# Kernel tuning notes

Measured on AMD Instinct MI355X. Metric: run time of the kernel, lower is better.

Reference implementation:

```python
import jax, jax.numpy as jnp
import numpy as np

N, H, CIN, C, G = 50000, 16, 256, 256, 8
CPG = C // G          # 32 channels per group
CR = C // 4           # delta MLP hidden (delta_reduction=4)

def _lrelu(x):
    return jax.nn.leaky_relu(x, 0.1)

def setup_inputs() -> dict:
    key = jax.random.key(0)
    ks = jax.random.split(key, 16)
    def lin(k, fin, fout):
        return jax.random.normal(k, (fin, fout), jnp.float32) / np.sqrt(fin)
    return {
        'q_pts': jax.random.normal(ks[0], (N, 3), jnp.float32),
        's_pts': jax.random.normal(ks[1], (N, 3), jnp.float32),
        's_feats': jax.random.normal(ks[2], (N, CIN), jnp.float32),
        'neighb_inds': jax.random.randint(ks[3], (N, H), 0, N, jnp.int64),
        'Wq': lin(ks[4], CIN, C), 'bq': jnp.zeros((C,), jnp.float32),
        'Wk': lin(ks[5], CIN, C), 'bk': jnp.zeros((C,), jnp.float32),
        'Wv': lin(ks[6], CIN, C), 'bv': jnp.zeros((C,), jnp.float32),
        'Wd1': lin(ks[7], 3, CR), 'bd1': jnp.zeros((CR,), jnp.float32),
        'Wd2': lin(ks[8], CR, C), 'bd2': jnp.zeros((C,), jnp.float32),
        'Wa1': lin(ks[9], C, CPG), 'ba1': jnp.zeros((CPG,), jnp.float32),
        'Wa2': lin(ks[10], CPG, CPG), 'ba2': jnp.zeros((CPG,), jnp.float32),
    }

def reference(q_pts, s_pts, s_feats, neighb_inds,
              Wq, bq, Wk, bk, Wv, bv,
              Wd1, bd1, Wd2, bd2, Wa1, ba1, Wa2, ba2):
    # q/k/v projections  (N, C)
    v = s_feats @ Wv + bv
    k = s_feats @ Wk + bk
    q = s_feats @ Wq + bq
    # gather neighbor features (all indices < N, shadow mask is a no-op)
    nv = v[neighb_inds]                 # (N, H, C)
    nk = k[neighb_inds]                 # (N, H, C)
    # relative positions (torch.no_grad in source)
    rel = s_pts[neighb_inds] - q_pts[:, None, :]   # (N, H, 3)
    # delta MLP: 3 -> C/4 -> C (UnaryBlock + Linear, norm='none')
    geom = _lrelu(rel @ Wd1 + bd1) @ Wd2 + bd2     # (N, H, C)
    # geom_mode='sub': v-branch and qk-branch both subtract geom encodings
    nv = nv - geom
    # source always enters strided branch (s_pts padded before the check);
    # stride_mode='nearest' -> q feature of the first neighbor
    qf = q[neighb_inds[:, 0]]                      # (N, C)
    qk = qf[:, None, :] - nk - geom                # (N, H, C)
    # alpha MLP: NormBlock(id) + act, Linear C->CpG + act, Linear CpG->CpG
    a = _lrelu(qk)
    a = _lrelu(a @ Wa1 + ba1)
    a = a @ Wa2 + ba2                              # (N, H, CpG)
    attn = jax.nn.softmax(a, axis=1)               # softmax over neighbors
    # grouped weighted aggregation: C split as (CpG, G), attn broadcast over G
    out = (nv.reshape(N, H, CPG, G) * attn[..., None]).sum(axis=1)
    return out.reshape(N, C)
```

## Files before the change

### kernel.cpp

```cpp
#include <hip/hip_runtime.h>
#include <cstdint>
#include <cstddef>

#define N_PTS 50000
#define H 16
#define CIN 256
#define C 256
#define CPG 32
#define CR 64

typedef short bf16x8 __attribute__((ext_vector_type(8)));
typedef float f32x4 __attribute__((ext_vector_type(4)));

__device__ __forceinline__ unsigned short f2bf(float f) {
    unsigned int u = __float_as_uint(f);
    u += 0x7fff + ((u >> 16) & 1);
    return (unsigned short)(u >> 16);
}
__device__ __forceinline__ float bf2f(unsigned short s) {
    return __uint_as_float(((unsigned int)s) << 16);
}

__global__ __launch_bounds__(256) void prep_all(
    const float* __restrict__ feats,
    const float* __restrict__ Wq, const float* __restrict__ Wk,
    const float* __restrict__ Wv,
    const float* __restrict__ Wd2, const float* __restrict__ Wa1,
    const float* __restrict__ Wa2,
    unsigned short* __restrict__ A_bf16,
    unsigned short* __restrict__ gemmFrags,
    unsigned short* __restrict__ attnFrags)
{
    int bid = blockIdx.x;
    if (bid < 6250) {
        size_t i = ((size_t)bid * 256 + threadIdx.x) * 8;
        float4 f0 = *(const float4*)&feats[i];
        float4 f1 = *(const float4*)&feats[i + 4];
        unsigned short t[8] = {f2bf(f0.x), f2bf(f0.y), f2bf(f0.z), f2bf(f0.w),
                               f2bf(f1.x), f2bf(f1.y), f2bf(f1.z), f2bf(f1.w)};
        *(bf16x8*)&A_bf16[i] = *(bf16x8*)t;
    } else if (bid < 6346) {
        int t = (bid - 6250) * 256 + threadIdx.x;
        int lane = t & 63;
        int f = t >> 6;
        int ntg = f % 48;
        const float* W = ntg < 16 ? Wq : (ntg < 32 ? Wk : Wv);
        int colc = (ntg & 15) * 16 + (lane & 15);
        int row0 = (f / 48) * 32 + ((lane >> 4) << 3);
        unsigned short tmp[8];
        #pragma unroll
        for (int j = 0; j < 8; ++j) tmp[j] = f2bf(W[(size_t)(row0 + j) * 256 + colc]);
        *(bf16x8*)&gemmFrags[(size_t)t * 8] = *(bf16x8*)tmp;
    } else {
        int t = (bid - 6346) * 256 + threadIdx.x;
        if (t >= 3200) return;
        const float* W; int Nc, NT, loc, base;
        if (t < 2048)      { W = Wd2; Nc = 256; NT = 16; loc = t;        base = 0; }
        else if (t < 3072) { W = Wa1; Nc = 32;  NT = 2;  loc = t - 2048; base = 16384; }
        else               { W = Wa2; Nc = 32;  NT = 2;  loc = t - 3072; base = 24576; }
        int f = loc >> 6, lane = loc & 63;
        int kt = f / NT, nt = f - kt * NT;
        int colc = nt * 16 + (lane & 15);
        int row0 = kt * 32 + ((lane >> 4) << 3);
        unsigned short tmp[8];
        #pragma unroll
        for (int j = 0; j < 8; ++j) tmp[j] = f2bf(W[(size_t)(row0 + j) * Nc + colc]);
        *(bf16x8*)&attnFrags[(size_t)(base + loc * 8)] = *(bf16x8*)tmp;
    }
}

__global__ __launch_bounds__(256) void qkv_gemm_mfma(
    const unsigned short* __restrict__ A,
    const unsigned short* __restrict__ wfrags,
    const float* __restrict__ bq, const float* __restrict__ bk,
    const float* __restrict__ bv, unsigned short* __restrict__ out)
{
    const int tid = threadIdx.x;
    const int lane = tid & 63, wave = tid >> 6;
    const int quad = lane >> 4, col16 = lane & 15;
    const int bx = blockIdx.x, by = blockIdx.y;

    int r0 = by * 128 + wave * 32 + col16;
    int r1 = r0 + 16;
    r0 = r0 < N_PTS ? r0 : N_PTS - 1;
    r1 = r1 < N_PTS ? r1 : N_PTS - 1;
    const unsigned short* a0p = &A[(size_t)r0 * 256 + quad * 8];
    const unsigned short* a1p = &A[(size_t)r1 * 256 + quad * 8];
    const unsigned short* bp  = &wfrags[(((size_t)bx * 8) * 64 + lane) * 8];

    f32x4 acc[2][8] = {};

    #pragma unroll 2
    for (int kt = 0; kt < 8; ++kt) {
        bf16x8 af0 = *(const bf16x8*)(a0p + kt * 32);
        bf16x8 af1 = *(const bf16x8*)(a1p + kt * 32);
        const unsigned short* bkt = bp + (size_t)kt * 48 * 64 * 8;
        #pragma unroll
        for (int nt = 0; nt < 8; ++nt) {
            bf16x8 bf = *(const bf16x8*)(bkt + (size_t)nt * 64 * 8);
            acc[0][nt] = __builtin_amdgcn_mfma_f32_16x16x32_bf16(af0, bf, acc[0][nt], 0, 0, 0);
            acc[1][nt] = __builtin_amdgcn_mfma_f32_16x16x32_bf16(af1, bf, acc[1][nt], 0, 0, 0);
        }
    }

    const int mode = bx >> 1;
    const float* bias = mode == 0 ? bq : (mode == 1 ? bk : bv);
    #pragma unroll
    for (int nt = 0; nt < 8; ++nt) {
        int cIn = (bx & 1) * 128 + nt * 16 + col16;
        float bb = bias[cIn];
        int pos = mode == 0 ? cIn : (256 + 2 * cIn + (mode == 2 ? 1 : 0));
        #pragma unroll
        for (int mt = 0; mt < 2; ++mt) {
            #pragma unroll
            for (int r = 0; r < 4; ++r) {
                int row = by * 128 + wave * 32 + mt * 16 + quad * 4 + r;
                if (row < N_PTS)
                    out[(size_t)row * 768 + pos] = f2bf(acc[mt][nt][r] + bb);
            }
        }
    }
}

#define D1S 72
#define PGS 66
#define QKS 264
#define A1S 40
#define A2S 33

__global__ __launch_bounds__(256, 3) void attn_mfma(
    const unsigned short* __restrict__ qkv,
    const float* __restrict__ q_pts, const float* __restrict__ s_pts,
    const int* __restrict__ nbr,
    const float* __restrict__ Wd1, const float* __restrict__ bd1,
    const float* __restrict__ bd2,
    const unsigned short* __restrict__ frags,
    const float* __restrict__ ba1, const float* __restrict__ ba2,
    float* __restrict__ out)
{
    __shared__ unsigned short s_d1[H * D1S];
    __shared__ float          s_pg[4 * H * PGS];
    __shared__ unsigned short s_qk[H * QKS];
    __shared__ unsigned short s_a1[H * A1S];
    __shared__ float          s_a2[H * A2S];
    __shared__ float          s_rel[4][H][3];
    __shared__ int            s_idx[4][H];

    const int tid = threadIdx.x;
    const int lane = tid & 63, wave = tid >> 6;
    const int quad = lane >> 4, col = lane & 15;
    const int n0 = blockIdx.x * 4;
    const int c = tid;

    if (tid < 64) {
        int pp = tid >> 4, hh = tid & 15;
        int idx = nbr[(size_t)(n0 + pp) * H + hh];
        s_idx[pp][hh] = idx;
        #pragma unroll
        for (int x = 0; x < 3; ++x)
            s_rel[pp][hh][x] = s_pts[(size_t)idx * 3 + x] - q_pts[(size_t)(n0 + pp) * 3 + x];
    }

    const float w1x = Wd1[lane], w1y = Wd1[64 + lane], w1z = Wd1[128 + lane];
    const float b1 = bd1[lane];
    const float b2 = bd2[c];
    bf16x8 wd2f[2][4];
    #pragma unroll
    for (int t = 0; t < 4; ++t) {
        wd2f[0][t] = *(const bf16x8*)&frags[((size_t)((0 * 16 + wave * 4 + t) * 64 + lane)) * 8];
        wd2f[1][t] = *(const bf16x8*)&frags[((size_t)((1 * 16 + wave * 4 + t) * 64 + lane)) * 8];
    }
    bf16x8 wa1f[8];
    bf16x8 wa2f = {0,0,0,0,0,0,0,0};
    if (wave < 2) {
        #pragma unroll
        for (int kt = 0; kt < 8; ++kt)
            wa1f[kt] = *(const bf16x8*)&frags[16384 + ((size_t)((kt * 2 + wave) * 64 + lane)) * 8];
        wa2f = *(const bf16x8*)&frags[24576 + ((size_t)(wave * 64 + lane)) * 8];
    }
    __syncthreads();

    float* pg = &s_pg[wave * (H * PGS)];

    for (int p = 0; p < 4; ++p) {
        const int n = n0 + p;

        #pragma unroll
        for (int pass = 0; pass < 4; ++pass) {
            int h = pass * 4 + wave;
            float v = b1 + s_rel[p][h][0] * w1x + s_rel[p][h][1] * w1y + s_rel[p][h][2] * w1z;
            s_d1[h * D1S + lane] = f2bf(fmaxf(v, 0.1f * v));
        }
        __syncthreads();

        unsigned int u[H];
        #pragma unroll
        for (int h = 0; h < H; ++h)
            u[h] = *(const unsigned int*)&qkv[(size_t)s_idx[p][h] * 768 + 256 + 2 * c];
        float qf = bf2f(qkv[(size_t)s_idx[p][0] * 768 + c]);

        {
            bf16x8 ga = *(bf16x8*)&s_d1[col * D1S + quad * 8];
            bf16x8 gb = *(bf16x8*)&s_d1[col * D1S + 32 + quad * 8];
            #pragma unroll
            for (int t = 0; t < 4; ++t) {
                f32x4 acc = {0.f, 0.f, 0.f, 0.f};
                acc = __builtin_amdgcn_mfma_f32_16x16x32_bf16(ga, wd2f[0][t], acc, 0, 0, 0);
                acc = __builtin_amdgcn_mfma_f32_16x16x32_bf16(gb, wd2f[1][t], acc, 0, 0, 0);
                #pragma unroll
                for (int rr = 0; rr < 4; ++rr)
                    pg[(quad * 4 + rr) * PGS + t * 16 + col] = acc[rr];
            }
        }

        float vg[H];
        #pragma unroll
        for (int h = 0; h < H; ++h) {
            float g = pg[h * PGS + lane] + b2;
            float nk = __uint_as_float(u[h] << 16);
            float nv = __uint_as_float(u[h] & 0xffff0000u);
            vg[h] = nv - g;
            float tq = qf - nk - g;
            s_qk[h * QKS + c] = f2bf(fmaxf(tq, 0.1f * tq));
        }
        __syncthreads();

        if (wave < 2) {
            f32x4 acc = {0.f, 0.f, 0.f, 0.f};
            #pragma unroll
            for (int kt = 0; kt < 8; ++kt) {
                bf16x8 a = *(bf16x8*)&s_qk[col * QKS + kt * 32 + quad * 8];
                acc = __builtin_amdgcn_mfma_f32_16x16x32_bf16(a, wa1f[kt], acc, 0, 0, 0);
            }
            int j = wave * 16 + col;
            float bb = ba1[j];
            #pragma unroll
            for (int rr = 0; rr < 4; ++rr) {
                float v = acc[rr] + bb;
                s_a1[(quad * 4 + rr) * A1S + j] = f2bf(fmaxf(v, 0.1f * v));
            }
        }
        __syncthreads();

        if (wave < 2) {
            bf16x8 aa = *(bf16x8*)&s_a1[col * A1S + quad * 8];
            f32x4 acc = {0.f, 0.f, 0.f, 0.f};
            acc = __builtin_amdgcn_mfma_f32_16x16x32_bf16(aa, wa2f, acc, 0, 0, 0);
            int j = wave * 16 + col;
            float bb = ba2[j];
            #pragma unroll
            for (int rr = 0; rr < 4; ++rr)
                s_a2[(quad * 4 + rr) * A2S + j] = acc[rr] + bb;
        }
        __syncthreads();

        if (wave == 0) {
            int j = lane & 31, hb = (lane >> 5) * 8;
            float vals[8];
            float mx = -1e30f;
            #pragma unroll
            for (int i = 0; i < 8; ++i) {
                vals[i] = s_a2[(hb + i) * A2S + j];
                mx = fmaxf(mx, vals[i]);
            }
            mx = fmaxf(mx, __shfl_xor(mx, 32));
            float sum = 0.f;
            #pragma unroll
            for (int i = 0; i < 8; ++i) { vals[i] = __expf(vals[i] - mx); sum += vals[i]; }
            sum += __shfl_xor(sum, 32);
            float inv = 1.f / sum;
            #pragma unroll
            for (int i = 0; i < 8; ++i) s_a2[(hb + i) * A2S + j] = vals[i] * inv;
        }
        __syncthreads();

        float o = 0.f;
        const int aj = c >> 3;
        #pragma unroll
        for (int h = 0; h < H; ++h) o += vg[h] * s_a2[h * A2S + aj];
        out[(size_t)n * C + c] = o;
    }
}


extern "C" void kernel_launch(void* const* d_in, const int* in_sizes, int n_in,
                              void* d_out, int out_size, void* d_ws, size_t ws_size,
                              hipStream_t stream) {
    const float* q_pts   = (const float*)d_in[0];
    const float* s_pts   = (const float*)d_in[1];
    const float* s_feats = (const float*)d_in[2];
    const int*   nbr     = (const int*)d_in[3];
    const float* Wq  = (const float*)d_in[4];
    const float* bq  = (const float*)d_in[5];
    const float* Wk  = (const float*)d_in[6];
    const float* bk  = (const float*)d_in[7];
    const float* Wv  = (const float*)d_in[8];
    const float* bv  = (const float*)d_in[9];
    const float* Wd1 = (const float*)d_in[10];
    const float* bd1 = (const float*)d_in[11];
    const float* Wd2 = (const float*)d_in[12];
    const float* bd2 = (const float*)d_in[13];
    const float* Wa1 = (const float*)d_in[14];
    const float* ba1 = (const float*)d_in[15];
    const float* Wa2 = (const float*)d_in[16];
    const float* ba2 = (const float*)d_in[17];

    float* out = (float*)d_out;
    char* ws = (char*)d_ws;
    unsigned short* A_bf16    = (unsigned short*)(ws);
    unsigned short* qkvb      = (unsigned short*)(ws + 25600000);
    unsigned short* attnFrags = (unsigned short*)(ws + 102400000);
    unsigned short* gemmFrags = (unsigned short*)(ws + 102451200);

    prep_all<<<6359, 256, 0, stream>>>(s_feats, Wq, Wk, Wv, Wd2, Wa1, Wa2,
                                       A_bf16, gemmFrags, attnFrags);

    dim3 g1(6, (N_PTS + 127) / 128);
    qkv_gemm_mfma<<<g1, 256, 0, stream>>>(A_bf16, gemmFrags, bq, bk, bv, qkvb);

    attn_mfma<<<(N_PTS / 4), 256, 0, stream>>>(qkvb, q_pts, s_pts, nbr,
                                               Wd1, bd1, bd2, attnFrags,
                                               ba1, ba2, out);
}
```

Before: 412.6 us.

## Prefetch next point's neighbor K/V gathers and use LDS-only barriers in attention kernel

```diff
diff --git a/kernel.cpp b/kernel.cpp
--- a/kernel.cpp
+++ b/kernel.cpp
@@ -20,6 +20,10 @@
 __device__ __forceinline__ float bf2f(unsigned short s) {
     return __uint_as_float(((unsigned int)s) << 16);
 }
+
+#define LBAR() do { asm volatile("s_waitcnt lgkmcnt(0)" ::: "memory"); \
+                    __builtin_amdgcn_s_barrier();                      \
+                    asm volatile("" ::: "memory"); } while (0)
 
 __global__ __launch_bounds__(256) void prep_all(
     const float* __restrict__ feats,
@@ -128,7 +132,7 @@
 #define A1S 40
 #define A2S 33
 
-__global__ __launch_bounds__(256, 3) void attn_mfma(
+__global__ __launch_bounds__(256, 4) void attn_mfma(
     const unsigned short* __restrict__ qkv,
     const float* __restrict__ q_pts, const float* __restrict__ s_pts,
     const int* __restrict__ nbr,
@@ -138,7 +142,7 @@
     const float* __restrict__ ba1, const float* __restrict__ ba2,
     float* __restrict__ out)
 {
-    __shared__ unsigned short s_d1[H * D1S];
+    __shared__ unsigned short s_d1[4 * H * D1S];
     __shared__ float          s_pg[4 * H * PGS];
     __shared__ unsigned short s_qk[H * QKS];
     __shared__ unsigned short s_a1[H * A1S];
@@ -180,28 +184,33 @@
     }
     __syncthreads();
 
-    float* pg = &s_pg[wave * (H * PGS)];
-
+    unsigned int u[H];
+    float qfv;
+    #pragma unroll
+    for (int h = 0; h < H; ++h)
+        u[h] = *(const unsigned int*)&qkv[(size_t)s_idx[0][h] * 768 + 256 + 2 * c];
+    qfv = bf2f(qkv[(size_t)s_idx[0][0] * 768 + c]);
+
+    #pragma unroll
     for (int p = 0; p < 4; ++p) {
-        const int n = n0 + p;
-
         #pragma unroll
         for (int pass = 0; pass < 4; ++pass) {
             int h = pass * 4 + wave;
             float v = b1 + s_rel[p][h][0] * w1x + s_rel[p][h][1] * w1y + s_rel[p][h][2] * w1z;
-            s_d1[h * D1S + lane] = f2bf(fmaxf(v, 0.1f * v));
-        }
-        __syncthreads();
-
-        unsigned int u[H];
-        #pragma unroll
-        for (int h = 0; h < H; ++h)
-            u[h] = *(const unsigned int*)&qkv[(size_t)s_idx[p][h] * 768 + 256 + 2 * c];
-        float qf = bf2f(qkv[(size_t)s_idx[p][0] * 768 + c]);
+            s_d1[(p * H + h) * D1S + lane] = f2bf(fmaxf(v, 0.1f * v));
+        }
+    }
+    LBAR();
+
+    float* pg = &s_pg[wave * (H * PGS)];
+
+    for (int p = 0; p < 4; ++p) {
+        const int n = n0 + p;
+        const unsigned short* d1p = &s_d1[p * H * D1S];
 
         {
-            bf16x8 ga = *(bf16x8*)&s_d1[col * D1S + quad * 8];
-            bf16x8 gb = *(bf16x8*)&s_d1[col * D1S + 32 + quad * 8];
+            bf16x8 ga = *(bf16x8*)&d1p[col * D1S + quad * 8];
+            bf16x8 gb = *(bf16x8*)&d1p[col * D1S + 32 + quad * 8];
             #pragma unroll
             for (int t = 0; t < 4; ++t) {
                 f32x4 acc = {0.f, 0.f, 0.f, 0.f};
@@ -220,10 +229,18 @@
             float nk = __uint_as_float(u[h] << 16);
             float nv = __uint_as_float(u[h] & 0xffff0000u);
             vg[h] = nv - g;
-            float tq = qf - nk - g;
+            float tq = qfv - nk - g;
             s_qk[h * QKS + c] = f2bf(fmaxf(tq, 0.1f * tq));
         }
-        __syncthreads();
+
+        if (p < 3) {
+            #pragma unroll
+            for (int h = 0; h < H; ++h)
+                u[h] = *(const unsigned int*)&qkv[(size_t)s_idx[p + 1][h] * 768 + 256 + 2 * c];
+            qfv = bf2f(qkv[(size_t)s_idx[p + 1][0] * 768 + c]);
+        }
+
+        LBAR();
 
         if (wave < 2) {
             f32x4 acc = {0.f, 0.f, 0.f, 0.f};
@@ -240,7 +257,7 @@
                 s_a1[(quad * 4 + rr) * A1S + j] = f2bf(fmaxf(v, 0.1f * v));
             }
         }
-        __syncthreads();
+        LBAR();
 
         if (wave < 2) {
             bf16x8 aa = *(bf16x8*)&s_a1[col * A1S + quad * 8];
@@ -252,7 +269,7 @@
             for (int rr = 0; rr < 4; ++rr)
                 s_a2[(quad * 4 + rr) * A2S + j] = acc[rr] + bb;
         }
-        __syncthreads();
+        LBAR();
 
         if (wave == 0) {
             int j = lane & 31, hb = (lane >> 5) * 8;
@@ -272,7 +289,7 @@
             #pragma unroll
             for (int i = 0; i < 8; ++i) s_a2[(hb + i) * A2S + j] = vals[i] * inv;
         }
-        __syncthreads();
+        LBAR();
 
         float o = 0.f;
         const int aj = c >> 3;
```

Result: slower. 605.5 us (+46.8%).
